# Kernel optimization log

Measured on AMD Instinct MI355X. Metric: run time of the kernel, lower is better.

## Reference

```python
import math
import jax, jax.numpy as jnp
import numpy as np

B, S, D, H = 2, 2048, 1024, 16
DH = D // H
EPS = 1e-5


def setup_inputs() -> dict:
    key = jax.random.key(0)
    ks = jax.random.split(key, 8)
    def lin(k, din, dout):
        return jax.random.normal(k, (din, dout), dtype=jnp.float32) / math.sqrt(din)
    return {
        "x": jax.random.normal(ks[0], (B, S, D), dtype=jnp.float32),
        "attention_mask": jnp.ones((B, S), dtype=jnp.int32),
        "Wq": lin(ks[1], D, D),
        "Wk": lin(ks[2], D, D),
        "Wv": lin(ks[3], D, D),
        "Wo": lin(ks[4], D, D),
        "W1": lin(ks[5], D, 4 * D),
        "W2": lin(ks[6], 2 * D, D),
        "gamma1": jnp.ones((D,), jnp.float32),
        "beta1": jnp.zeros((D,), jnp.float32),
        "gamma2": jnp.ones((D,), jnp.float32),
        "beta2": jnp.zeros((D,), jnp.float32),
    }


def layernorm(x, gamma, beta):
    mu = jnp.mean(x, axis=-1, keepdims=True)
    xc = x - mu
    var = jnp.mean(xc * xc, axis=-1, keepdims=True)
    return gamma * (xc / jnp.sqrt(var + EPS)) + beta


def softmax_last(x):
    x = x - jnp.max(x, axis=-1, keepdims=True)
    e = jnp.exp(x)
    return e / jnp.sum(e, axis=-1, keepdims=True)


def mhsa(x, attention_mask, Wq, Wk, Wv, Wo, causal=True):
    b, s, d = x.shape
    q = (x @ Wq).reshape(b, s, H, DH).transpose(0, 2, 1, 3)  # [b,h,s,dh]
    k = (x @ Wk).reshape(b, s, H, DH).transpose(0, 2, 1, 3)
    v = (x @ Wv).reshape(b, s, H, DH).transpose(0, 2, 1, 3)
    score = jnp.einsum("bhqd,bhkd->bhqk", q, k) / math.sqrt(DH)
    if causal:
        cmask = jnp.tril(jnp.ones((s, s), dtype=bool))
        score = jnp.where(cmask[None, None], score, -jnp.inf)
    key_mask = attention_mask.astype(bool)[:, None, None, :]  # [b,1,1,s]
    score = jnp.where(key_mask, score, -jnp.inf)
    attn = softmax_last(score)
    out = jnp.einsum("bhqk,bhkd->bhqd", attn, v)
    out = out.transpose(0, 2, 1, 3).reshape(b, s, d)
    return out @ Wo


def reference(x, attention_mask, Wq, Wk, Wv, Wo, W1, W2, gamma1, beta1, gamma2, beta2):
    x1 = x + mhsa(layernorm(x, gamma1, beta1), attention_mask, Wq, Wk, Wv, Wo, causal=True)
    h = layernorm(x1, gamma2, beta2) @ W1          # [b,s,4d]
    left, right = h[:, :, : 2 * D], h[:, :, 2 * D :]
    glu = left * jax.nn.sigmoid(right)             # [b,s,2d]
    return x1 + glu @ W2
```

## Files before the change

kernel.cpp:

```cpp
#include <hip/hip_runtime.h>
#include <hip/hip_bf16.h>
#include <math.h>

#define BB 2
#define SS 2048
#define DD 1024
#define HH 16
#define DH 64
#define NTOK (BB * SS)
#define LN_EPS 1e-5f
#define BIGNEG -1e30f

typedef __attribute__((ext_vector_type(8))) short bf16x8;
typedef __attribute__((ext_vector_type(4))) float f32x4;

static __device__ __forceinline__ unsigned short f2bu(float f) {
    __hip_bfloat16 h = __float2bfloat16(f);
    return *(unsigned short*)&h;
}

static __device__ __forceinline__ void async16(const void* g, void* l) {
    __builtin_amdgcn_global_load_lds((const __attribute__((address_space(1))) void*)g,
                                     (__attribute__((address_space(3))) void*)l, 16, 0, 0);
}


__global__ __launch_bounds__(256) void prep_kernel(const float* __restrict__ Wq,
                                                   const float* __restrict__ Wk,
                                                   const float* __restrict__ Wv,
                                                   const float* __restrict__ Wo,
                                                   const float* __restrict__ W1,
                                                   const float* __restrict__ W2,
                                                   __hip_bfloat16* __restrict__ wqkvt,
                                                   __hip_bfloat16* __restrict__ wot,
                                                   __hip_bfloat16* __restrict__ w1t,
                                                   __hip_bfloat16* __restrict__ w2t,
                                                   const float* __restrict__ x,
                                                   const float* __restrict__ gamma,
                                                   const float* __restrict__ beta,
                                                   __hip_bfloat16* __restrict__ lnb) {
    __shared__ float t[32][33];
    __shared__ float red[256];
    const int bid = blockIdx.x;
    const int tid = threadIdx.x;

    if (bid >= 10240) {
        const int row = bid - 10240;
        const float* xp = x + (size_t)row * DD;
        float vals[4];
        float s = 0.f;
#pragma unroll
        for (int i = 0; i < 4; ++i) {
            float v = xp[tid + i * 256];
            vals[i] = v;
            s += v;
        }
        red[tid] = s;
        __syncthreads();
        for (int st = 128; st > 0; st >>= 1) {
            if (tid < st) red[tid] += red[tid + st];
            __syncthreads();
        }
        const float mu = red[0] * (1.0f / DD);
        __syncthreads();
        float sq = 0.f;
#pragma unroll
        for (int i = 0; i < 4; ++i) {
            float d = vals[i] - mu;
            sq += d * d;
        }
        red[tid] = sq;
        __syncthreads();
        for (int st = 128; st > 0; st >>= 1) {
            if (tid < st) red[tid] += red[tid + st];
            __syncthreads();
        }
        const float rinv = rsqrtf(red[0] * (1.0f / DD) + LN_EPS);
        __hip_bfloat16* op = lnb + (size_t)row * DD;
#pragma unroll
        for (int i = 0; i < 4; ++i) {
            int j = tid + i * 256;
            op[j] = __float2bfloat16(gamma[j] * ((vals[i] - mu) * rinv) + beta[j]);
        }
        return;
    }

    const float* W;
    __hip_bfloat16* Wt;
    int K, N, tile;
    if (bid < 4096) {
        const int m = bid >> 10;
        tile = bid & 1023;
        W = (m == 0) ? Wq : (m == 1) ? Wk : (m == 2) ? Wv : Wo;
        Wt = (m < 3) ? (wqkvt + (size_t)m * 1024 * 1024) : wot;
        K = 1024; N = 1024;
    } else if (bid < 8192) {
        tile = bid - 4096; W = W1; Wt = w1t; K = 1024; N = 4096;
    } else {
        tile = bid - 8192; W = W2; Wt = w2t; K = 2048; N = 1024;
    }
    const int nt = N >> 5;
    const int n0 = (tile % nt) * 32, k0 = (tile / nt) * 32;
    const int tx = tid & 31, ty = tid >> 5;
#pragma unroll
    for (int i = 0; i < 4; ++i)
        t[ty + 8 * i][tx] = W[(size_t)(k0 + ty + 8 * i) * N + n0 + tx];
    __syncthreads();
#pragma unroll
    for (int i = 0; i < 4; ++i)
        Wt[(size_t)(n0 + ty + 8 * i) * K + k0 + tx] = __float2bfloat16(t[tx][ty + 8 * i]);
}

__global__ __launch_bounds__(256) void ln_kernel(const float* __restrict__ x,
                                                 const float* __restrict__ gamma,
                                                 const float* __restrict__ beta,
                                                 __hip_bfloat16* __restrict__ out) {
    const int row = blockIdx.x;
    const int tid = threadIdx.x;
    __shared__ float red[256];

    const float* xp = x + (size_t)row * DD;
    float vals[4];
    float s = 0.f;
#pragma unroll
    for (int i = 0; i < 4; ++i) {
        float v = xp[tid + i * 256];
        vals[i] = v;
        s += v;
    }
    red[tid] = s;
    __syncthreads();
    for (int st = 128; st > 0; st >>= 1) {
        if (tid < st) red[tid] += red[tid + st];
        __syncthreads();
    }
    const float mu = red[0] * (1.0f / DD);
    __syncthreads();
    float sq = 0.f;
#pragma unroll
    for (int i = 0; i < 4; ++i) {
        float d = vals[i] - mu;
        sq += d * d;
    }
    red[tid] = sq;
    __syncthreads();
    for (int st = 128; st > 0; st >>= 1) {
        if (tid < st) red[tid] += red[tid + st];
        __syncthreads();
    }
    const float rinv = rsqrtf(red[0] * (1.0f / DD) + LN_EPS);

    __hip_bfloat16* op = out + (size_t)row * DD;
#pragma unroll
    for (int i = 0; i < 4; ++i) {
        int j = tid + i * 256;
        op[j] = __float2bfloat16(gamma[j] * ((vals[i] - mu) * rinv) + beta[j]);
    }
}

__global__ __launch_bounds__(256) void vtrans(const __hip_bfloat16* __restrict__ qkvb_,
                                              __hip_bfloat16* __restrict__ VT_) {
    const unsigned short* src = (const unsigned short*)qkvb_;
    unsigned short* dst = (unsigned short*)VT_;
    __shared__ unsigned short t[64][65];
    const int c0 = (blockIdx.x & 15) << 6;
    const int t0 = (blockIdx.x >> 4) << 6;
    const int tx = threadIdx.x & 63, ty = threadIdx.x >> 6;
#pragma unroll
    for (int i = 0; i < 16; ++i)
        t[ty + 4 * i][tx] = src[(size_t)(t0 + ty + 4 * i) * 3072 + 2048 + c0 + tx];
    __syncthreads();
#pragma unroll
    for (int i = 0; i < 16; ++i)
        dst[(size_t)(c0 + ty + 4 * i) * 4096 + t0 + tx] = t[tx][ty + 4 * i];
}

template <int RES, int EPI>
__global__ __launch_bounds__(256) void mfma_gemm(const __hip_bfloat16* __restrict__ A,
                                                 const __hip_bfloat16* __restrict__ Bt,
                                                 const void* __restrict__ res,
                                                 void* __restrict__ out,
                                                 int M, int N, int K,
                                                 int xcdCols, int colGroups) {
    __shared__ short As[128 * 64];
    __shared__ short Bs[128 * 64];
    const int tid = threadIdx.x;
    const int lane = tid & 63;
    const int wave = tid >> 6;
    const int xcd = blockIdx.x & 7;
    const int i = blockIdx.x >> 3;
    const int xcdRows = (gridDim.x >> 3) / xcdCols;
    const int r = i / xcdCols;
    const int c = i - r * xcdCols;
    const int rowg = xcd / colGroups;
    const int colg = xcd - rowg * colGroups;
    const int row0 = (rowg * xcdRows + r) * 128;
    const int col0 = (colg * xcdCols + c) * 128;
    const int wr = (wave >> 1) * 64;
    const int wc = (wave & 1) * 64;
    const int l15 = lane & 15;
    const int quad = lane >> 4;
    const int s7 = l15 & 7;

    f32x4 acc[4][4] = {};

    for (int k0 = 0; k0 < K; k0 += 64) {
#pragma unroll
        for (int rr = 0; rr < 4; ++rr) {
            const int ec = rr * 256 + tid;
            const int ar = ec >> 3, d = ec & 7;
            const int ao = (d ^ (ar & 7)) << 3;
            async16(&A[(size_t)(row0 + ar) * K + k0 + ao], &As[ec << 3]);
            async16(&Bt[(size_t)(col0 + ar) * K + k0 + ao], &Bs[ec << 3]);
        }
        __syncthreads();
#pragma unroll
        for (int kk = 0; kk < 2; ++kk) {
            const int co = (((kk << 2) | quad) ^ s7) << 3;
            bf16x8 af[4], bfr[4];
#pragma unroll
            for (int ii = 0; ii < 4; ++ii)
                af[ii] = *(const bf16x8*)&As[(wr + ii * 16 + l15) * 64 + co];
#pragma unroll
            for (int j = 0; j < 4; ++j)
                bfr[j] = *(const bf16x8*)&Bs[(wc + j * 16 + l15) * 64 + co];
#pragma unroll
            for (int ii = 0; ii < 4; ++ii)
#pragma unroll
                for (int j = 0; j < 4; ++j)
                    acc[ii][j] = __builtin_amdgcn_mfma_f32_16x16x32_bf16(af[ii], bfr[j], acc[ii][j], 0, 0, 0);
        }
        __syncthreads();
    }

    const int r4 = quad * 4;
#pragma unroll
    for (int ii = 0; ii < 4; ++ii) {
#pragma unroll
        for (int j = 0; j < 4; ++j) {
            const int orow0 = row0 + wr + ii * 16 + r4;
            const int ocol = col0 + wc + j * 16 + l15;
#pragma unroll
            for (int rg = 0; rg < 4; ++rg) {
                const size_t oi = (size_t)(orow0 + rg) * N + ocol;
                float v = acc[ii][j][rg];
                if constexpr (RES == 1) v += ((const float*)res)[oi];
                if constexpr (EPI == 0) ((float*)out)[oi] = v;
                if constexpr (EPI == 1) ((__hip_bfloat16*)out)[oi] = __float2bfloat16(v);
            }
        }
    }
}

template <int RES, int EPI>
__global__ __launch_bounds__(256) void mfma_gemm_n64(const __hip_bfloat16* __restrict__ A,
                                                     const __hip_bfloat16* __restrict__ Bt,
                                                     const void* __restrict__ res,
                                                     void* __restrict__ out,
                                                     int N, int K, int colTiles) {
    __shared__ short As[128 * 64];
    __shared__ short Bs[64 * 64];
    const int tid = threadIdx.x;
    const int lane = tid & 63;
    const int wave = tid >> 6;
    const int cpx = gridDim.x >> 3;
    const int wg = (blockIdx.x & 7) * cpx + (blockIdx.x >> 3);
    const int row0 = (wg / colTiles) * 128;
    const int col0 = (wg % colTiles) * 64;
    const int wr = wave * 32;
    const int l15 = lane & 15;
    const int quad = lane >> 4;
    const int s7 = l15 & 7;

    f32x4 acc[2][4] = {};

    for (int k0 = 0; k0 < K; k0 += 64) {
#pragma unroll
        for (int r = 0; r < 4; ++r) {
            const int ec = r * 256 + tid;
            const int ar = ec >> 3, d = ec & 7;
            const int ao = (d ^ (ar & 7)) << 3;
            async16(&A[(size_t)(row0 + ar) * K + k0 + ao], &As[ec << 3]);
        }
#pragma unroll
        for (int r = 0; r < 2; ++r) {
            const int ec = r * 256 + tid;
            const int ar = ec >> 3, d = ec & 7;
            const int ao = (d ^ (ar & 7)) << 3;
            async16(&Bt[(size_t)(col0 + ar) * K + k0 + ao], &Bs[ec << 3]);
        }
        __syncthreads();
#pragma unroll
        for (int kk = 0; kk < 2; ++kk) {
            const int co = (((kk << 2) | quad) ^ s7) << 3;
            bf16x8 af[2], bfr[4];
#pragma unroll
            for (int i = 0; i < 2; ++i)
                af[i] = *(const bf16x8*)&As[(wr + i * 16 + l15) * 64 + co];
#pragma unroll
            for (int j = 0; j < 4; ++j)
                bfr[j] = *(const bf16x8*)&Bs[(j * 16 + l15) * 64 + co];
#pragma unroll
            for (int i = 0; i < 2; ++i)
#pragma unroll
                for (int j = 0; j < 4; ++j)
                    acc[i][j] = __builtin_amdgcn_mfma_f32_16x16x32_bf16(af[i], bfr[j], acc[i][j], 0, 0, 0);
        }
        __syncthreads();
    }

    const int r4 = quad * 4;
#pragma unroll
    for (int i = 0; i < 2; ++i) {
#pragma unroll
        for (int j = 0; j < 4; ++j) {
            const int orow0 = row0 + wr + i * 16 + r4;
            const int ocol = col0 + j * 16 + l15;
#pragma unroll
            for (int rg = 0; rg < 4; ++rg) {
                const size_t oi = (size_t)(orow0 + rg) * N + ocol;
                float v = acc[i][j][rg];
                if constexpr (RES == 1) v += ((const float*)res)[oi];
                if constexpr (EPI == 0) ((float*)out)[oi] = v;
                if constexpr (EPI == 1) ((__hip_bfloat16*)out)[oi] = __float2bfloat16(v);
            }
        }
    }
}

__global__ __launch_bounds__(256) void mfma_gemm_glu64(const __hip_bfloat16* __restrict__ A,
                                                       const __hip_bfloat16* __restrict__ Bt,
                                                       __hip_bfloat16* __restrict__ out) {
    __shared__ short As[128 * 64];
    __shared__ short Bl[64 * 64];
    __shared__ short Br[64 * 64];
    const int tid = threadIdx.x;
    const int lane = tid & 63;
    const int wave = tid >> 6;
    const int xcd = blockIdx.x & 7;
    const int i = blockIdx.x >> 3;
    const int row0 = ((xcd >> 1) * 8 + (i >> 4)) * 128;
    const int col0 = ((xcd & 1) * 16 + (i & 15)) * 64;
    const int wr = wave * 32;
    const int l15 = lane & 15;
    const int quad = lane >> 4;
    const int s7 = l15 & 7;

    f32x4 accl[2][4] = {};
    f32x4 accr[2][4] = {};

    for (int k0 = 0; k0 < 1024; k0 += 64) {
#pragma unroll
        for (int r = 0; r < 4; ++r) {
            const int ec = r * 256 + tid;
            const int ar = ec >> 3, d = ec & 7;
            const int ao = (d ^ (ar & 7)) << 3;
            async16(&A[(size_t)(row0 + ar) * 1024 + k0 + ao], &As[ec << 3]);
        }
#pragma unroll
        for (int r = 0; r < 2; ++r) {
            const int ec = r * 256 + tid;
            const int ar = ec >> 3, d = ec & 7;
            const int ao = (d ^ (ar & 7)) << 3;
            async16(&Bt[(size_t)(col0 + ar) * 1024 + k0 + ao], &Bl[ec << 3]);
            async16(&Bt[(size_t)(2048 + col0 + ar) * 1024 + k0 + ao], &Br[ec << 3]);
        }
        __syncthreads();
#pragma unroll
        for (int kk = 0; kk < 2; ++kk) {
            const int co = (((kk << 2) | quad) ^ s7) << 3;
            bf16x8 af[2], bl[4], br[4];
#pragma unroll
            for (int ii = 0; ii < 2; ++ii)
                af[ii] = *(const bf16x8*)&As[(wr + ii * 16 + l15) * 64 + co];
#pragma unroll
            for (int j = 0; j < 4; ++j) {
                bl[j] = *(const bf16x8*)&Bl[(j * 16 + l15) * 64 + co];
                br[j] = *(const bf16x8*)&Br[(j * 16 + l15) * 64 + co];
            }
#pragma unroll
            for (int ii = 0; ii < 2; ++ii)
#pragma unroll
                for (int j = 0; j < 4; ++j) {
                    accl[ii][j] = __builtin_amdgcn_mfma_f32_16x16x32_bf16(af[ii], bl[j], accl[ii][j], 0, 0, 0);
                    accr[ii][j] = __builtin_amdgcn_mfma_f32_16x16x32_bf16(af[ii], br[j], accr[ii][j], 0, 0, 0);
                }
        }
        __syncthreads();
    }

    const int r4 = quad * 4;
#pragma unroll
    for (int ii = 0; ii < 2; ++ii) {
#pragma unroll
        for (int j = 0; j < 4; ++j) {
#pragma unroll
            for (int rg = 0; rg < 4; ++rg) {
                const int orow = row0 + wr + ii * 16 + r4 + rg;
                const int ocol = col0 + j * 16 + l15;
                const float l = accl[ii][j][rg];
                const float r = accr[ii][j][rg];
                out[(size_t)orow * 2048 + ocol] =
                    __float2bfloat16(l * (1.f / (1.f + __expf(-r))));
            }
        }
    }
}

#define KADV (64 * 3072)
#define RESCALE_THR 8.f

__global__ __launch_bounds__(256, 4) void flash_mfma(const __hip_bfloat16* __restrict__ qkv_,
                                                     const __hip_bfloat16* __restrict__ VT_,
                                                     const int* __restrict__ mask,
                                                     __hip_bfloat16* __restrict__ attnb) {
    const unsigned short* qkv = (const unsigned short*)qkv_;
    const unsigned short* VT = (const unsigned short*)VT_;
    __shared__ __align__(16) short Ks[2][64 * 64];
    __shared__ __align__(16) short Vt[2][64 * 64];
    __shared__ __align__(16) short Ps[4][16 * 64];

    const int tid = threadIdx.x;
    const int lane = tid & 63;
    const int wave = tid >> 6;
    const int l15 = lane & 15;
    const int quad = lane >> 4;
    const int s7 = l15 & 7;

    const int xcd = blockIdx.x & 7;
    const int slot = blockIdx.x >> 3;
    const int bh = xcd + ((slot & 3) << 3);
    const int v = slot >> 2;
    const int vr = v & 7, vs = v >> 3;
    const int qt = (vs == 0) ? 31 - vr : (vs == 1) ? vr : (vs == 2) ? 23 - vr : 8 + vr;
    const int h = bh & 15;
    const int b = bh >> 4;
    const int q0 = qt * 64 + wave * 16;

    const int e0 = tid, e1 = 256 + tid;
    const int r0 = e0 >> 3, d0 = e0 & 7, r1 = e1 >> 3, d1 = e1 & 7;
    const unsigned short* kp0 = qkv + (size_t)(b * SS + r0) * 3072 + 1024 + h * 64 + ((d0 ^ (r0 & 7)) << 3);
    const unsigned short* kp1 = qkv + (size_t)(b * SS + r1) * 3072 + 1024 + h * 64 + ((d1 ^ (r1 & 7)) << 3);
    const unsigned short* vp0 = VT + (size_t)(h * 64 + r0) * 4096 + b * SS + ((d0 ^ (r0 & 7)) << 3);
    const unsigned short* vp1 = VT + (size_t)(h * 64 + r1) * 4096 + b * SS + ((d1 ^ (r1 & 7)) << 3);
    short* const kd0a = &Ks[0][e0 << 3]; short* const kd0b = &Ks[1][e0 << 3];
    short* const kd1a = &Ks[0][e1 << 3]; short* const kd1b = &Ks[1][e1 << 3];
    short* const vd0a = &Vt[0][e0 << 3]; short* const vd0b = &Vt[1][e0 << 3];
    short* const vd1a = &Vt[0][e1 << 3]; short* const vd1b = &Vt[1][e1 << 3];

    const int* const mrow = mask + b * SS;

    bf16x8 aq[2];
#pragma unroll
    for (int ks = 0; ks < 2; ++ks)
        aq[ks] = *(const bf16x8*)(qkv + (size_t)(b * SS + q0 + l15) * 3072 +
                                  h * 64 + ks * 32 + quad * 8);

    f32x4 O[4];
#pragma unroll
    for (int i = 0; i < 4; ++i) O[i] = (f32x4){0.f, 0.f, 0.f, 0.f};
    float m_r = BIGNEG, l_r = 0.f;

    short* const Pw = &Ps[wave][0];

    async16(kp0, kd0a); async16(kp1, kd1a);
    async16(vp0, vd0a); async16(vp1, vd1a);
    kp0 += KADV; kp1 += KADV; vp0 += 64; vp1 += 64;

    for (int c = 0; c < qt; ++c) {
        const int cur = c & 1;
        __syncthreads();

        async16(kp0, cur ? kd0a : kd0b);
        async16(kp1, cur ? kd1a : kd1b);
        async16(vp0, cur ? vd0a : vd0b);
        async16(vp1, cur ? vd1a : vd1b);
        kp0 += KADV; kp1 += KADV; vp0 += 64; vp1 += 64;

        const int kb = c << 6;
        const short* Kc = &Ks[cur][0];
        const short* Vc = &Vt[cur][0];

        int4 mv[4];
#pragma unroll
        for (int kt = 0; kt < 4; ++kt)
            mv[kt] = *(const int4*)&mrow[kb + kt * 16 + quad * 4];

        f32x4 S[4];
        __builtin_amdgcn_s_setprio(1);
#pragma unroll
        for (int kt = 0; kt < 4; ++kt) {
            const bf16x8 bk0 = *(const bf16x8*)&Kc[(kt * 16 + l15) * 64 + ((quad ^ s7) << 3)];
            const bf16x8 bk1 = *(const bf16x8*)&Kc[(kt * 16 + l15) * 64 + (((4 | quad) ^ s7) << 3)];
            f32x4 z = {0.f, 0.f, 0.f, 0.f};
            z = __builtin_amdgcn_mfma_f32_16x16x32_bf16(bk0, aq[0], z, 0, 0, 0);
            S[kt] = __builtin_amdgcn_mfma_f32_16x16x32_bf16(bk1, aq[1], z, 0, 0, 0);
        }
        __builtin_amdgcn_s_setprio(0);

#pragma unroll
        for (int kt = 0; kt < 4; ++kt) {
            const int* mm = (const int*)&mv[kt];
#pragma unroll
            for (int rg = 0; rg < 4; ++rg)
                S[kt][rg] = fmaf(S[kt][rg], 0.125f, mm[rg] ? 0.f : BIGNEG);
        }

        const float t0 = fmaxf(fmaxf(S[0][0], S[0][1]), fmaxf(S[0][2], S[0][3]));
        const float t1 = fmaxf(fmaxf(S[1][0], S[1][1]), fmaxf(S[1][2], S[1][3]));
        const float t2 = fmaxf(fmaxf(S[2][0], S[2][1]), fmaxf(S[2][2], S[2][3]));
        const float t3 = fmaxf(fmaxf(S[3][0], S[3][1]), fmaxf(S[3][2], S[3][3]));
        float tmax = fmaxf(fmaxf(t0, t1), fmaxf(t2, t3));
        tmax = fmaxf(tmax, __shfl_xor(tmax, 16));
        tmax = fmaxf(tmax, __shfl_xor(tmax, 32));

        if (__any(tmax > m_r + RESCALE_THR)) {
            const float mn = fmaxf(m_r, tmax);
            const float alpha = __expf(m_r - mn);
            m_r = mn;
            l_r *= alpha;
#pragma unroll
            for (int nt = 0; nt < 4; ++nt)
#pragma unroll
                for (int rg = 0; rg < 4; ++rg)
                    O[nt][rg] *= alpha;
        }

        float rsum = 0.f;
        unsigned long long p64[4];
#pragma unroll
        for (int kt = 0; kt < 4; ++kt) {
#pragma unroll
            for (int rg = 0; rg < 4; ++rg)
                S[kt][rg] = __expf(S[kt][rg] - m_r);
            rsum += (S[kt][0] + S[kt][1]) + (S[kt][2] + S[kt][3]);
            p64[kt] = ((unsigned long long)(((unsigned)f2bu(S[kt][3]) << 16) | f2bu(S[kt][2])) << 32)
                    | (((unsigned)f2bu(S[kt][1]) << 16) | f2bu(S[kt][0]));
        }
        rsum += __shfl_xor(rsum, 16);
        rsum += __shfl_xor(rsum, 32);
        l_r += rsum;

#pragma unroll
        for (int kt = 0; kt < 4; ++kt) {
            const int ch = (kt << 1) | (quad >> 1);
            const int base = (l15 << 6) + ((ch ^ s7) << 3) + ((quad & 1) << 2);
            *(unsigned long long*)&Pw[base] = p64[kt];
        }

        __builtin_amdgcn_s_setprio(1);
#pragma unroll
        for (int kk = 0; kk < 2; ++kk) {
            const int co = ((((kk << 2) | quad) ^ s7) << 3);
            const bf16x8 bp = *(const bf16x8*)&Pw[(l15 << 6) + co];
#pragma unroll
            for (int nt = 0; nt < 4; ++nt) {
                const bf16x8 av = *(const bf16x8*)&Vc[(nt * 16 + l15) * 64 + co];
                O[nt] = __builtin_amdgcn_mfma_f32_16x16x32_bf16(av, bp, O[nt], 0, 0, 0);
            }
        }
        __builtin_amdgcn_s_setprio(0);
    }

    {
        const int cur = qt & 1;
        __syncthreads();

        const int kb = qt << 6;
        const int ktmax = wave + 1;
        const int ktfull = wave;
        const short* Kc = &Ks[cur][0];
        const short* Vc = &Vt[cur][0];
        const int qrow = q0 + l15;

        int4 mv[4];
#pragma unroll
        for (int kt = 0; kt < 4; ++kt) {
            if (kt >= ktmax) break;
            mv[kt] = *(const int4*)&mrow[kb + kt * 16 + quad * 4];
        }

        f32x4 S[4];
        __builtin_amdgcn_s_setprio(1);
#pragma unroll
        for (int kt = 0; kt < 4; ++kt) {
            if (kt >= ktmax) break;
            const bf16x8 bk0 = *(const bf16x8*)&Kc[(kt * 16 + l15) * 64 + ((quad ^ s7) << 3)];
            const bf16x8 bk1 = *(const bf16x8*)&Kc[(kt * 16 + l15) * 64 + (((4 | quad) ^ s7) << 3)];
            f32x4 z = {0.f, 0.f, 0.f, 0.f};
            z = __builtin_amdgcn_mfma_f32_16x16x32_bf16(bk0, aq[0], z, 0, 0, 0);
            S[kt] = __builtin_amdgcn_mfma_f32_16x16x32_bf16(bk1, aq[1], z, 0, 0, 0);
        }
        __builtin_amdgcn_s_setprio(0);

#pragma unroll
        for (int kt = 0; kt < 4; ++kt) {
            if (kt >= ktmax) break;
            const int* mm = (const int*)&mv[kt];
#pragma unroll
            for (int rg = 0; rg < 4; ++rg) {
                float s = fmaf(S[kt][rg], 0.125f, mm[rg] ? 0.f : BIGNEG);
                if (kt >= ktfull) {
                    const int key = kb + kt * 16 + quad * 4 + rg;
                    s = (key <= qrow) ? s : BIGNEG;
                }
                S[kt][rg] = s;
            }
        }

        float tmax = BIGNEG;
#pragma unroll
        for (int kt = 0; kt < 4; ++kt) {
            if (kt >= ktmax) break;
            tmax = fmaxf(tmax, fmaxf(fmaxf(S[kt][0], S[kt][1]),
                                     fmaxf(S[kt][2], S[kt][3])));
        }
        tmax = fmaxf(tmax, __shfl_xor(tmax, 16));
        tmax = fmaxf(tmax, __shfl_xor(tmax, 32));

        if (__any(tmax > m_r + RESCALE_THR)) {
            const float mn = fmaxf(m_r, tmax);
            const float alpha = __expf(m_r - mn);
            m_r = mn;
            l_r *= alpha;
#pragma unroll
            for (int nt = 0; nt < 4; ++nt)
#pragma unroll
                for (int rg = 0; rg < 4; ++rg)
                    O[nt][rg] *= alpha;
        }

        float rsum = 0.f;
#pragma unroll
        for (int kt = 0; kt < 4; ++kt) {
            if (kt >= ktmax) break;
#pragma unroll
            for (int rg = 0; rg < 4; ++rg)
                S[kt][rg] = __expf(S[kt][rg] - m_r);
            rsum += (S[kt][0] + S[kt][1]) + (S[kt][2] + S[kt][3]);
            const int ch = (kt << 1) | (quad >> 1);
            const int base = (l15 << 6) + ((ch ^ s7) << 3) + ((quad & 1) << 2);
            *(unsigned long long*)&Pw[base] =
                ((unsigned long long)(((unsigned)f2bu(S[kt][3]) << 16) | f2bu(S[kt][2])) << 32)
                | (((unsigned)f2bu(S[kt][1]) << 16) | f2bu(S[kt][0]));
        }
        rsum += __shfl_xor(rsum, 16);
        rsum += __shfl_xor(rsum, 32);
        l_r += rsum;

        const int kkmax = (ktmax + 1) >> 1;
        if (ktmax & 1) {
            const int ch = (ktmax << 1) | (quad >> 1);
            const int base = (l15 << 6) + ((ch ^ s7) << 3) + ((quad & 1) << 2);
            *(unsigned long long*)&Pw[base] = 0ull;
        }

        __builtin_amdgcn_s_setprio(1);
#pragma unroll
        for (int kk = 0; kk < 2; ++kk) {
            if (kk >= kkmax) break;
            const int co = ((((kk << 2) | quad) ^ s7) << 3);
            const bf16x8 bp = *(const bf16x8*)&Pw[(l15 << 6) + co];
#pragma unroll
            for (int nt = 0; nt < 4; ++nt) {
                const bf16x8 av = *(const bf16x8*)&Vc[(nt * 16 + l15) * 64 + co];
                O[nt] = __builtin_amdgcn_mfma_f32_16x16x32_bf16(av, bp, O[nt], 0, 0, 0);
            }
        }
        __builtin_amdgcn_s_setprio(0);
    }

    const float inv = 1.f / l_r;
    unsigned short* op = (unsigned short*)attnb +
                         (size_t)(b * SS + q0 + l15) * 1024 + h * 64 + quad * 4;
#pragma unroll
    for (int nt = 0; nt < 4; ++nt) {
        const float o0 = O[nt][0] * inv, o1 = O[nt][1] * inv;
        const float o2 = O[nt][2] * inv, o3 = O[nt][3] * inv;
        const unsigned long long pk =
            (unsigned long long)(((unsigned)f2bu(o3) << 16) | f2bu(o2)) << 32 |
            (((unsigned)f2bu(o1) << 16) | f2bu(o0));
        *(unsigned long long*)(op + nt * 16) = pk;
    }
}

extern "C" void kernel_launch(void* const* d_in, const int* in_sizes, int n_in,
                              void* d_out, int out_size, void* d_ws, size_t ws_size,
                              hipStream_t stream) {
    const float* x  = (const float*)d_in[0];
    const int* mask = (const int*)d_in[1];
    const float* Wq = (const float*)d_in[2];
    const float* Wk = (const float*)d_in[3];
    const float* Wv = (const float*)d_in[4];
    const float* Wo = (const float*)d_in[5];
    const float* W1 = (const float*)d_in[6];
    const float* W2 = (const float*)d_in[7];
    const float* g1 = (const float*)d_in[8];
    const float* b1 = (const float*)d_in[9];
    const float* g2 = (const float*)d_in[10];
    const float* b2 = (const float*)d_in[11];

    const size_t MB = 1024 * 1024;
    uint8_t* ws = (uint8_t*)d_ws;
    __hip_bfloat16* wqkvt = (__hip_bfloat16*)(ws);
    __hip_bfloat16* wot   = (__hip_bfloat16*)(ws + 6 * MB);
    __hip_bfloat16* w1t   = (__hip_bfloat16*)(ws + 8 * MB);
    __hip_bfloat16* w2t   = (__hip_bfloat16*)(ws + 16 * MB);
    __hip_bfloat16* lnb   = (__hip_bfloat16*)(ws + 20 * MB);
    __hip_bfloat16* qkvb  = (__hip_bfloat16*)(ws + 28 * MB);
    float*          x1    = (float*)(ws + 28 * MB);
    __hip_bfloat16* attnb = (__hip_bfloat16*)(ws + 52 * MB);
    __hip_bfloat16* VT    = (__hip_bfloat16*)(ws + 60 * MB);
    __hip_bfloat16* glub  = (__hip_bfloat16*)(ws + 68 * MB);

    prep_kernel<<<10240 + NTOK, 256, 0, stream>>>(Wq, Wk, Wv, Wo, W1, W2,
                                                  wqkvt, wot, w1t, w2t,
                                                  x, g1, b1, lnb);

    mfma_gemm<0, 1><<<768, 256, 0, stream>>>(lnb, wqkvt, nullptr, qkvb,
                                             NTOK, 3072, 1024, 12, 2);

    vtrans<<<1024, 256, 0, stream>>>(qkvb, VT);

    flash_mfma<<<1024, 256, 0, stream>>>(qkvb, VT, mask, attnb);

    mfma_gemm_n64<1, 0><<<512, 256, 0, stream>>>(attnb, wot, x, x1, 1024, 1024, 16);

    ln_kernel<<<NTOK, 256, 0, stream>>>(x1, g2, b2, lnb);

    mfma_gemm_glu64<<<1024, 256, 0, stream>>>(lnb, w1t, glub);

    mfma_gemm_n64<1, 0><<<512, 256, 0, stream>>>(glub, w2t, x1, (float*)d_out,
                                                 1024, 2048, 16);
}
```

Baseline: 194.6 us.

## Fuse V transpose into QKV GEMM epilogue and interleave W1 for GLU

The QKV GEMM epilogue now writes V tiles straight into the transposed VT buffer as packed bf16x4 stores, so the separate vtrans kernel and its extra read/write of V are gone. W1 columns are interleaved (left/right alternating) during weight prep, which lets the GLU GEMM use the standard 128x128 tile with 4x4 MFMA accumulators and pair left/right values via a lane shuffle in the epilogue. This aims to cut a kernel launch plus memory traffic and to raise MFMA reuse in the GLU GEMM. In exchange, half the lanes idle during the GLU store and the VT writes are strided 8-byte stores.

```diff
diff --git a/kernel.cpp b/kernel.cpp
--- a/kernel.cpp
+++ b/kernel.cpp
@@ -88,6 +88,7 @@
     const float* W;
     __hip_bfloat16* Wt;
     int K, N, tile;
+    bool ilv = false;
     if (bid < 4096) {
         const int m = bid >> 10;
         tile = bid & 1023;
@@ -96,6 +97,7 @@
         K = 1024; N = 1024;
     } else if (bid < 8192) {
         tile = bid - 4096; W = W1; Wt = w1t; K = 1024; N = 4096;
+        ilv = true;
     } else {
         tile = bid - 8192; W = W2; Wt = w2t; K = 2048; N = 1024;
     }
@@ -107,8 +109,11 @@
         t[ty + 8 * i][tx] = W[(size_t)(k0 + ty + 8 * i) * N + n0 + tx];
     __syncthreads();
 #pragma unroll
-    for (int i = 0; i < 4; ++i)
-        Wt[(size_t)(n0 + ty + 8 * i) * K + k0 + tx] = __float2bfloat16(t[tx][ty + 8 * i]);
+    for (int i = 0; i < 4; ++i) {
+        const int n = n0 + ty + 8 * i;
+        const int rn = ilv ? ((n < 2048) ? (n << 1) : (((n - 2048) << 1) | 1)) : n;
+        Wt[(size_t)rn * K + k0 + tx] = __float2bfloat16(t[tx][ty + 8 * i]);
+    }
 }
 
 __global__ __launch_bounds__(256) void ln_kernel(const float* __restrict__ x,
@@ -158,30 +163,14 @@
     }
 }
 
-__global__ __launch_bounds__(256) void vtrans(const __hip_bfloat16* __restrict__ qkvb_,
-                                              __hip_bfloat16* __restrict__ VT_) {
-    const unsigned short* src = (const unsigned short*)qkvb_;
-    unsigned short* dst = (unsigned short*)VT_;
-    __shared__ unsigned short t[64][65];
-    const int c0 = (blockIdx.x & 15) << 6;
-    const int t0 = (blockIdx.x >> 4) << 6;
-    const int tx = threadIdx.x & 63, ty = threadIdx.x >> 6;
-#pragma unroll
-    for (int i = 0; i < 16; ++i)
-        t[ty + 4 * i][tx] = src[(size_t)(t0 + ty + 4 * i) * 3072 + 2048 + c0 + tx];
-    __syncthreads();
-#pragma unroll
-    for (int i = 0; i < 16; ++i)
-        dst[(size_t)(c0 + ty + 4 * i) * 4096 + t0 + tx] = t[tx][ty + 4 * i];
-}
-
 template <int RES, int EPI>
 __global__ __launch_bounds__(256) void mfma_gemm(const __hip_bfloat16* __restrict__ A,
                                                  const __hip_bfloat16* __restrict__ Bt,
                                                  const void* __restrict__ res,
                                                  void* __restrict__ out,
                                                  int M, int N, int K,
-                                                 int xcdCols, int colGroups) {
+                                                 int xcdCols, int colGroups,
+                                                 __hip_bfloat16* __restrict__ vtout) {
     __shared__ short As[128 * 64];
     __shared__ short Bs[128 * 64];
     const int tid = threadIdx.x;
@@ -234,6 +223,21 @@
     }
 
     const int r4 = quad * 4;
+    if (vtout != nullptr && col0 >= 2048) {
+#pragma unroll
+        for (int ii = 0; ii < 4; ++ii) {
+#pragma unroll
+            for (int j = 0; j < 4; ++j) {
+                const int cc = col0 + wc + j * 16 + l15 - 2048;
+                const int orow0 = row0 + wr + ii * 16 + r4;
+                const unsigned long long pk =
+                    (unsigned long long)(((unsigned)f2bu(acc[ii][j][3]) << 16) | f2bu(acc[ii][j][2])) << 32 |
+                    (((unsigned)f2bu(acc[ii][j][1]) << 16) | f2bu(acc[ii][j][0]));
+                *(unsigned long long*)((unsigned short*)vtout + (size_t)cc * 4096 + orow0) = pk;
+            }
+        }
+        return;
+    }
 #pragma unroll
     for (int ii = 0; ii < 4; ++ii) {
 #pragma unroll
@@ -328,80 +332,71 @@
     }
 }
 
-__global__ __launch_bounds__(256) void mfma_gemm_glu64(const __hip_bfloat16* __restrict__ A,
-                                                       const __hip_bfloat16* __restrict__ Bt,
-                                                       __hip_bfloat16* __restrict__ out) {
+__global__ __launch_bounds__(256) void mfma_gemm_glu128(const __hip_bfloat16* __restrict__ A,
+                                                        const __hip_bfloat16* __restrict__ Bt,
+                                                        __hip_bfloat16* __restrict__ out) {
     __shared__ short As[128 * 64];
-    __shared__ short Bl[64 * 64];
-    __shared__ short Br[64 * 64];
+    __shared__ short Bs[128 * 64];
     const int tid = threadIdx.x;
     const int lane = tid & 63;
     const int wave = tid >> 6;
     const int xcd = blockIdx.x & 7;
     const int i = blockIdx.x >> 3;
     const int row0 = ((xcd >> 1) * 8 + (i >> 4)) * 128;
-    const int col0 = ((xcd & 1) * 16 + (i & 15)) * 64;
-    const int wr = wave * 32;
+    const int col0 = ((xcd & 1) * 16 + (i & 15)) * 128;
+    const int wr = (wave >> 1) * 64;
+    const int wc = (wave & 1) * 64;
     const int l15 = lane & 15;
     const int quad = lane >> 4;
     const int s7 = l15 & 7;
 
-    f32x4 accl[2][4] = {};
-    f32x4 accr[2][4] = {};
+    f32x4 acc[4][4] = {};
 
     for (int k0 = 0; k0 < 1024; k0 += 64) {
 #pragma unroll
-        for (int r = 0; r < 4; ++r) {
-            const int ec = r * 256 + tid;
+        for (int rr = 0; rr < 4; ++rr) {
+            const int ec = rr * 256 + tid;
             const int ar = ec >> 3, d = ec & 7;
             const int ao = (d ^ (ar & 7)) << 3;
             async16(&A[(size_t)(row0 + ar) * 1024 + k0 + ao], &As[ec << 3]);
-        }
-#pragma unroll
-        for (int r = 0; r < 2; ++r) {
-            const int ec = r * 256 + tid;
-            const int ar = ec >> 3, d = ec & 7;
-            const int ao = (d ^ (ar & 7)) << 3;
-            async16(&Bt[(size_t)(col0 + ar) * 1024 + k0 + ao], &Bl[ec << 3]);
-            async16(&Bt[(size_t)(2048 + col0 + ar) * 1024 + k0 + ao], &Br[ec << 3]);
+            async16(&Bt[(size_t)(col0 + ar) * 1024 + k0 + ao], &Bs[ec << 3]);
         }
         __syncthreads();
 #pragma unroll
         for (int kk = 0; kk < 2; ++kk) {
             const int co = (((kk << 2) | quad) ^ s7) << 3;
-            bf16x8 af[2], bl[4], br[4];
-#pragma unroll
-            for (int ii = 0; ii < 2; ++ii)
+            bf16x8 af[4], bfr[4];
+#pragma unroll
+            for (int ii = 0; ii < 4; ++ii)
                 af[ii] = *(const bf16x8*)&As[(wr + ii * 16 + l15) * 64 + co];
 #pragma unroll
-            for (int j = 0; j < 4; ++j) {
-                bl[j] = *(const bf16x8*)&Bl[(j * 16 + l15) * 64 + co];
-                br[j] = *(const bf16x8*)&Br[(j * 16 + l15) * 64 + co];
-            }
-#pragma unroll
-            for (int ii = 0; ii < 2; ++ii)
-#pragma unroll
-                for (int j = 0; j < 4; ++j) {
-                    accl[ii][j] = __builtin_amdgcn_mfma_f32_16x16x32_bf16(af[ii], bl[j], accl[ii][j], 0, 0, 0);
-                    accr[ii][j] = __builtin_amdgcn_mfma_f32_16x16x32_bf16(af[ii], br[j], accr[ii][j], 0, 0, 0);
+            for (int j = 0; j < 4; ++j)
+                bfr[j] = *(const bf16x8*)&Bs[(wc + j * 16 + l15) * 64 + co];
+#pragma unroll
+            for (int ii = 0; ii < 4; ++ii)
+#pragma unroll
+                for (int j = 0; j < 4; ++j)
+                    acc[ii][j] = __builtin_amdgcn_mfma_f32_16x16x32_bf16(af[ii], bfr[j], acc[ii][j], 0, 0, 0);
+        }
+        __syncthreads();
+    }
+
+    const int r4 = quad * 4;
+    const bool writer = (lane & 1) == 0;
+#pragma unroll
+    for (int ii = 0; ii < 4; ++ii) {
+#pragma unroll
+        for (int j = 0; j < 4; ++j) {
+            const int cc = (col0 + wc + j * 16 + l15) >> 1;
+            const int orow0 = row0 + wr + ii * 16 + r4;
+#pragma unroll
+            for (int rg = 0; rg < 4; ++rg) {
+                const float v = acc[ii][j][rg];
+                const float rv = __shfl_xor(v, 1);
+                if (writer) {
+                    const float g = v * (1.f / (1.f + __expf(-rv)));
+                    out[(size_t)(orow0 + rg) * 2048 + cc] = __float2bfloat16(g);
                 }
-        }
-        __syncthreads();
-    }
-
-    const int r4 = quad * 4;
-#pragma unroll
-    for (int ii = 0; ii < 2; ++ii) {
-#pragma unroll
-        for (int j = 0; j < 4; ++j) {
-#pragma unroll
-            for (int rg = 0; rg < 4; ++rg) {
-                const int orow = row0 + wr + ii * 16 + r4 + rg;
-                const int ocol = col0 + j * 16 + l15;
-                const float l = accl[ii][j][rg];
-                const float r = accr[ii][j][rg];
-                out[(size_t)orow * 2048 + ocol] =
-                    __float2bfloat16(l * (1.f / (1.f + __expf(-r))));
             }
         }
     }
@@ -718,9 +713,7 @@
                                                   x, g1, b1, lnb);
 
     mfma_gemm<0, 1><<<768, 256, 0, stream>>>(lnb, wqkvt, nullptr, qkvb,
-                                             NTOK, 3072, 1024, 12, 2);
-
-    vtrans<<<1024, 256, 0, stream>>>(qkvb, VT);
+                                             NTOK, 3072, 1024, 12, 2, VT);
 
     flash_mfma<<<1024, 256, 0, stream>>>(qkvb, VT, mask, attnb);
 
@@ -728,7 +721,7 @@
 
     ln_kernel<<<NTOK, 256, 0, stream>>>(x1, g2, b2, lnb);
 
-    mfma_gemm_glu64<<<1024, 256, 0, stream>>>(lnb, w1t, glub);
+    mfma_gemm_glu128<<<1024, 256, 0, stream>>>(lnb, w1t, glub);
 
     mfma_gemm_n64<1, 0><<<512, 256, 0, stream>>>(glub, w2t, x1, (float*)d_out,
                                                  1024, 2048, 16);
```

Result: slower. 202.8 us (+4.2%).
